# Kernel tuning notes

Hardware: AMD Instinct MI355X
Metric: run time of the kernel (lower is better)

The kernel has to match this reference:

```python
import jax, jax.numpy as jnp
import numpy as np

# Static per-expert capacities (tokens are laid out contiguously per expert)
CAPS = [1024, 512, 1024, 256, 1024, 512, 128, 1024, 512, 1024, 256, 512, 1024, 128, 64, 512]
TOTAL = sum(CAPS)  # 9536
E, H, I = 16, 1024, 4096
OFFSETS = np.concatenate([[0], np.cumsum(CAPS)])


def setup_inputs() -> dict:
    key = jax.random.key(0)
    ks = jax.random.split(key, 5)
    x = jax.random.normal(ks[0], (TOTAL, H), dtype=jnp.float32)
    W1 = jax.random.normal(ks[1], (E, I, H), dtype=jnp.float32) * 0.02
    b1 = jax.random.normal(ks[2], (E, I), dtype=jnp.float32) * 0.02
    W2 = jax.random.normal(ks[3], (E, H, I), dtype=jnp.float32) * 0.02
    b2 = jax.random.normal(ks[4], (E, H), dtype=jnp.float32) * 0.02
    return {"x": x, "W1": W1, "b1": b1, "W2": W2, "b2": b2}


def reference(x, W1, b1, W2, b2):
    # Grouped GEMM FFN: expert e processes rows [OFFSETS[e]:OFFSETS[e+1]]
    # out = gelu(x_e @ W1[e].T + b1[e]) @ W2[e].T + b2[e]
    outs = []
    for e in range(E):  # fixed, static loop over experts (capacities are static)
        xs = x[OFFSETS[e]:OFFSETS[e + 1]]                      # [cap_e, H]
        h = jax.nn.gelu(xs @ W1[e].T + b1[e], approximate=False)  # [cap_e, I]
        outs.append(h @ W2[e].T + b2[e])                       # [cap_e, H]
    return jnp.concatenate(outs, axis=0)                       # [TOTAL, H]
```

## Files before the change

kernel.cpp:

```cpp
#include <hip/hip_runtime.h>
#include <math.h>

typedef __attribute__((ext_vector_type(8))) short short8;
typedef __attribute__((ext_vector_type(4))) float f32x4;
typedef __attribute__((ext_vector_type(2))) unsigned int u32x2;

#define E_NUM 16
constexpr int CAPS[E_NUM] = {1024,512,1024,256,1024,512,128,1024,512,1024,256,512,1024,128,64,512};
constexpr int OFFS[E_NUM] = {0,1024,1536,2560,2816,3840,4352,4480,5504,6016,7040,7296,7808,8832,8960,9024};
constexpr int cdiv_(int a, int b){ return (a + b - 1) / b; }
constexpr int ilog2_(int v){ int l = 0; while ((1 << l) < v) ++l; return l; }

__device__ __forceinline__ unsigned int cvt_pk_bf16(float a, float b){
  unsigned int r;
  asm("v_cvt_pk_bf16_f32 %0, %1, %2" : "=v"(r) : "v"(a), "v"(b));
  return r;
}

typedef __attribute__((address_space(1))) const unsigned char gas_u8;
typedef __attribute__((address_space(3))) unsigned char las_u8;
__device__ __forceinline__ void gl_lds16(const void* g, void* l){
  __builtin_amdgcn_global_load_lds((gas_u8*)g, (las_u8*)l, 16, 0, 0);
}

__global__ __launch_bounds__(256) void cvt_bf16_kernel(const float* __restrict__ x,
                                                       unsigned short* __restrict__ xb, int n8)
{
  int i = blockIdx.x * blockDim.x + threadIdx.x;
  const int stride = gridDim.x * blockDim.x;
  for (; i < n8; i += stride) {
    f32x4 a = *reinterpret_cast<const f32x4*>(x + (size_t)i * 8);
    f32x4 b = *reinterpret_cast<const f32x4*>(x + (size_t)i * 8 + 4);
    u32x2 lo, hi;
    lo[0] = cvt_pk_bf16(a[0], a[1]); lo[1] = cvt_pk_bf16(a[2], a[3]);
    hi[0] = cvt_pk_bf16(b[0], b[1]); hi[1] = cvt_pk_bf16(b[2], b[3]);
    *reinterpret_cast<u32x2*>(xb + (size_t)i * 8)     = lo;
    *reinterpret_cast<u32x2*>(xb + (size_t)i * 8 + 4) = hi;
  }
}

template<bool A_GLDS, bool GELU_OUT, int TM, int NDIM, int KDIM, int LOG_GN, int NWG>
__global__ __launch_bounds__(256, 4)
void expert_gemm(const void* __restrict__ Av, const float* __restrict__ W,
                 const float* __restrict__ bias, void* __restrict__ Outv)
{
  constexpr int A_SZ = TM * 32;
  constexpr int B_SZ = 128 * 32;
  constexpr int GN   = 1 << LOG_GN;
  constexpr int MFR  = TM / 32;
  static_assert(NWG % 8 == 0, "grid must be divisible by 8 for XCD swizzle");
  static_assert(!GELU_OUT || 2 * (A_SZ + B_SZ) >= 128 * 128, "GELU transpose needs 32KB");

  __shared__ __align__(16) unsigned short smem[2 * A_SZ + 2 * B_SZ];

  const int tid  = threadIdx.x;
  const int braw = blockIdx.x;
  const int t = (braw & 7) * (NWG / 8) + (braw >> 3);

  int m0 = 0, n0 = 0, Me = 0, tok0 = 0;
  size_t wbase = 0, bbase = 0;
  {
    int acc0 = 0;
    #pragma unroll
    for (int i = 0; i < E_NUM; ++i) {
      const int mt  = cdiv_(CAPS[i], TM);
      const int lmt = ilog2_(mt);
      const int nb  = mt * (NDIM / 128);
      if (t >= acc0 && t < acc0 + nb) {
        const int loc = t - acc0;
        const int g   = loc >> (lmt + LOG_GN);
        const int rem = loc & ((mt << LOG_GN) - 1);
        m0   = (rem >> LOG_GN) * TM;
        n0   = ((g << LOG_GN) | (rem & (GN - 1))) * 128;
        Me   = CAPS[i];
        tok0 = OFFS[i];
        wbase = (size_t)i * NDIM * KDIM;
        bbase = (size_t)i * NDIM;
      }
      acc0 += nb;
    }
  }
  const float* Wb = W + wbase;

  const int lane = tid & 63;
  const int wv   = tid >> 6;
  const int sr   = tid >> 3;
  const int sc   = (tid & 7) * 8;
  const int spc  = sc ^ ((sr & 3) << 4);

  const unsigned short* Ah = (const unsigned short*)Av;
  const float*          Af = (const float*)Av;

  f32x4 ra[MFR]; f32x4 rb[4];

  auto loadB = [&](int kt) {
    const int k0 = kt * 32;
    #pragma unroll
    for (int i = 0; i < 4; ++i)
      rb[i] = *reinterpret_cast<const f32x4*>(Wb + (size_t)(n0 + sr + 32 * i) * KDIM + k0 + (sc >> 1));
  };
  auto writeB = [&](int buf) {
    char* bb = (char*)(smem + 2 * A_SZ + buf * B_SZ);
    #pragma unroll
    for (int i = 0; i < 4; ++i) {
      u32x2 p;
      p[0] = cvt_pk_bf16(rb[i][0], rb[i][1]);
      p[1] = cvt_pk_bf16(rb[i][2], rb[i][3]);
      *reinterpret_cast<u32x2*>(bb + (sr + 32 * i) * 64 + spc) = p;
    }
  };

  auto stageA_glds = [&](int buf, int kt) {
    constexpr int AI = TM / 64;
    const unsigned short* Ag = Ah + (size_t)(tok0 + m0) * KDIM + kt * 32;
    #pragma unroll
    for (int j = 0; j < AI; ++j) {
      const int rbase = wv * (AI * 16) + j * 16;
      const int r     = rbase + (lane >> 2);
      const int gblk  = (lane & 3) ^ (r & 3);
      gl_lds16((const void*)(Ag + (size_t)r * KDIM + gblk * 8),
               (void*)(smem + buf * A_SZ + rbase * 32));
    }
  };
  auto loadA_reg = [&](int kt) {
    const int k0 = kt * 32;
    #pragma unroll
    for (int i = 0; i < MFR; ++i)
      ra[i] = *reinterpret_cast<const f32x4*>(Af + (size_t)(tok0 + m0 + sr + 32 * i) * KDIM + k0 + (sc >> 1));
  };
  auto writeA_reg = [&](int buf) {
    char* ab = (char*)(smem + buf * A_SZ);
    #pragma unroll
    for (int i = 0; i < MFR; ++i) {
      u32x2 p;
      p[0] = cvt_pk_bf16(ra[i][0], ra[i][1]);
      p[1] = cvt_pk_bf16(ra[i][2], ra[i][3]);
      *reinterpret_cast<u32x2*>(ab + (sr + 32 * i) * 64 + spc) = p;
    }
  };

  const int wm   = (wv >> 1) * (TM / 2);
  const int wn   = (wv & 1) * 64;
  const int lrow = lane & 15;
  const int fcs  = ((lane >> 4) << 4) ^ ((lane & 3) << 4);

  f32x4 acc_[MFR][4];
  #pragma unroll
  for (int i = 0; i < MFR; ++i)
    #pragma unroll
    for (int j = 0; j < 4; ++j)
      acc_[i][j] = (f32x4){0.f, 0.f, 0.f, 0.f};

  loadB(0);
  if constexpr (A_GLDS) stageA_glds(0, 0); else { loadA_reg(0); writeA_reg(0); }
  writeB(0);
  __syncthreads();

  constexpr int NT = KDIM / 32;
  for (int kt = 0; kt < NT; ++kt) {
    const int cur = kt & 1;
    if (kt + 1 < NT) {
      loadB(kt + 1);
      if constexpr (A_GLDS) stageA_glds(cur ^ 1, kt + 1);
      else                  loadA_reg(kt + 1);
    }

    const char* ab = (const char*)(smem + cur * A_SZ);
    const char* bb = (const char*)(smem + 2 * A_SZ + cur * B_SZ);
    short8 afr[MFR], bfr[4];
    #pragma unroll
    for (int f = 0; f < MFR; ++f)
      afr[f] = *reinterpret_cast<const short8*>(ab + (wm + f * 16 + lrow) * 64 + fcs);
    #pragma unroll
    for (int f = 0; f < 4; ++f)
      bfr[f] = *reinterpret_cast<const short8*>(bb + (wn + f * 16 + lrow) * 64 + fcs);

    #pragma unroll
    for (int i = 0; i < MFR; ++i)
      #pragma unroll
      for (int j = 0; j < 4; ++j)
        acc_[i][j] = __builtin_amdgcn_mfma_f32_16x16x32_bf16(afr[i], bfr[j], acc_[i][j], 0, 0, 0);

    if (kt + 1 < NT) {
      writeB(cur ^ 1);
      if constexpr (!A_GLDS) writeA_reg(cur ^ 1);
    }
    __syncthreads();
  }

  float bv[4];
  #pragma unroll
  for (int f = 0; f < 4; ++f)
    bv[f] = bias[bbase + n0 + wn + f * 16 + lrow];

  if constexpr (GELU_OUT) {
    static_assert(TM == 128, "GELU path assumes 128-row tiles");
    unsigned short* hout = smem;
    #pragma unroll
    for (int i = 0; i < MFR; ++i) {
      const int rbase = wm + i * 16 + (lane >> 4) * 4;
      #pragma unroll
      for (int j = 0; j < 4; ++j) {
        #pragma unroll
        for (int jj = 0; jj < 4; ++jj) {
          float xv = acc_[i][j][jj] + bv[j];
          float g  = 0.5f * xv * (1.0f + erff(xv * 0.70710678118654752f));
          hout[(rbase + jj) * 128 + wn + j * 16 + lrow] = (unsigned short)(cvt_pk_bf16(g, g) & 0xFFFFu);
        }
      }
    }
    __syncthreads();
    unsigned short* Oh = (unsigned short*)Outv;
    #pragma unroll
    for (int it = 0; it < 8; ++it) {
      int row  = it * 16 + (tid >> 4);
      int c    = (tid & 15) * 8;
      int grow = m0 + row;
      if (grow < Me) {
        *reinterpret_cast<short8*>(Oh + (size_t)(tok0 + grow) * NDIM + n0 + c)
          = *reinterpret_cast<const short8*>(hout + row * 128 + c);
      }
    }
  } else {
    float* Of = (float*)Outv;
    #pragma unroll
    for (int i = 0; i < MFR; ++i) {
      const int rbase = wm + i * 16 + (lane >> 4) * 4;
      #pragma unroll
      for (int jj = 0; jj < 4; ++jj) {
        int grow = m0 + rbase + jj;
        if (grow < Me) {
          #pragma unroll
          for (int j = 0; j < 4; ++j) {
            Of[(size_t)(tok0 + grow) * NDIM + n0 + wn + j * 16 + lrow] = acc_[i][j][jj] + bv[j];
          }
        }
      }
    }
  }
}

extern "C" void kernel_launch(void* const* d_in, const int* in_sizes, int n_in,
                              void* d_out, int out_size, void* d_ws, size_t ws_size,
                              hipStream_t stream)
{
  const float* x  = (const float*)d_in[0];
  const float* W1 = (const float*)d_in[1];
  const float* b1 = (const float*)d_in[2];
  const float* W2 = (const float*)d_in[3];
  const float* b2 = (const float*)d_in[4];
  float* out = (float*)d_out;

  constexpr size_t H_BYTES  = (size_t)9536 * 4096 * 2;
  constexpr size_t XB_BYTES = (size_t)9536 * 1024 * 2;
  unsigned short* h  = (unsigned short*)d_ws;
  unsigned short* xb = (unsigned short*)((char*)d_ws + H_BYTES);

  const bool use_xb = ws_size >= H_BYTES + XB_BYTES;

  if (use_xb) {
    cvt_bf16_kernel<<<2048, 256, 0, stream>>>(x, xb, 9536 * 1024 / 8);
    expert_gemm<true, true, 128, 4096, 1024, 2, 75 * 32>
        <<<75 * 32, 256, 0, stream>>>((const void*)xb, W1, b1, (void*)h);
  } else {
    expert_gemm<false, true, 128, 4096, 1024, 2, 75 * 32>
        <<<75 * 32, 256, 0, stream>>>((const void*)x, W1, b1, (void*)h);
  }

  expert_gemm<true, false, 64, 1024, 4096, 0, 149 * 8>
      <<<149 * 8, 256, 0, stream>>>((const void*)h, W2, b2, (void*)out);
}
```

Measured before the change: 398.2 us.

## Split-K second expert GEMM with atomics and use cheaper sigmoid-form GELU

Splits the K dimension of the down-projection GEMM into two chunks processed by separate workgroups, accumulating into a zeroed output via atomic adds with the bias scaled per split. This raises the workgroup count to improve occupancy and load balance. It also replaces the erf-based GELU with a tanh-style approximation expressed as x*sigmoid, and raises the launch-bounds occupancy hint. The costs are an extra memset, atomic traffic, nondeterministic summation order, slightly approximate GELU, and possible register pressure.

Measured after the change: 403.5 us. No clear change (+1.3%).

```diff
diff --git a/kernel.cpp b/kernel.cpp
--- a/kernel.cpp
+++ b/kernel.cpp
@@ -39,8 +39,8 @@
   }
 }
 
-template<bool A_GLDS, bool GELU_OUT, int TM, int NDIM, int KDIM, int LOG_GN, int NWG>
-__global__ __launch_bounds__(256, 4)
+template<bool A_GLDS, bool GELU_OUT, int TM, int NDIM, int KDIM, int LOG_GN, int NWG, int KS>
+__global__ __launch_bounds__(256, 8)
 void expert_gemm(const void* __restrict__ Av, const float* __restrict__ W,
                  const float* __restrict__ bias, void* __restrict__ Outv)
 {
@@ -48,14 +48,21 @@
   constexpr int B_SZ = 128 * 32;
   constexpr int GN   = 1 << LOG_GN;
   constexpr int MFR  = TM / 32;
+  constexpr int NT   = KDIM / (KS * 32);
+  constexpr int NWG1 = NWG / KS;
   static_assert(NWG % 8 == 0, "grid must be divisible by 8 for XCD swizzle");
   static_assert(!GELU_OUT || 2 * (A_SZ + B_SZ) >= 128 * 128, "GELU transpose needs 32KB");
+  static_assert(!GELU_OUT || KS == 1, "GELU path is KS=1 only");
 
   __shared__ __align__(16) unsigned short smem[2 * A_SZ + 2 * B_SZ];
 
   const int tid  = threadIdx.x;
   const int braw = blockIdx.x;
   const int t = (braw & 7) * (NWG / 8) + (braw >> 3);
+
+  const int kc    = t / NWG1;
+  const int tt    = t % NWG1;
+  const int kbase = kc * (KDIM / KS);
 
   int m0 = 0, n0 = 0, Me = 0, tok0 = 0;
   size_t wbase = 0, bbase = 0;
@@ -66,8 +73,8 @@
       const int mt  = cdiv_(CAPS[i], TM);
       const int lmt = ilog2_(mt);
       const int nb  = mt * (NDIM / 128);
-      if (t >= acc0 && t < acc0 + nb) {
-        const int loc = t - acc0;
+      if (tt >= acc0 && tt < acc0 + nb) {
+        const int loc = tt - acc0;
         const int g   = loc >> (lmt + LOG_GN);
         const int rem = loc & ((mt << LOG_GN) - 1);
         m0   = (rem >> LOG_GN) * TM;
@@ -94,7 +101,7 @@
   f32x4 ra[MFR]; f32x4 rb[4];
 
   auto loadB = [&](int kt) {
-    const int k0 = kt * 32;
+    const int k0 = kbase + kt * 32;
     #pragma unroll
     for (int i = 0; i < 4; ++i)
       rb[i] = *reinterpret_cast<const f32x4*>(Wb + (size_t)(n0 + sr + 32 * i) * KDIM + k0 + (sc >> 1));
@@ -112,7 +119,7 @@
 
   auto stageA_glds = [&](int buf, int kt) {
     constexpr int AI = TM / 64;
-    const unsigned short* Ag = Ah + (size_t)(tok0 + m0) * KDIM + kt * 32;
+    const unsigned short* Ag = Ah + (size_t)(tok0 + m0) * KDIM + kbase + kt * 32;
     #pragma unroll
     for (int j = 0; j < AI; ++j) {
       const int rbase = wv * (AI * 16) + j * 16;
@@ -123,7 +130,7 @@
     }
   };
   auto loadA_reg = [&](int kt) {
-    const int k0 = kt * 32;
+    const int k0 = kbase + kt * 32;
     #pragma unroll
     for (int i = 0; i < MFR; ++i)
       ra[i] = *reinterpret_cast<const f32x4*>(Af + (size_t)(tok0 + m0 + sr + 32 * i) * KDIM + k0 + (sc >> 1));
@@ -151,12 +158,29 @@
     for (int j = 0; j < 4; ++j)
       acc_[i][j] = (f32x4){0.f, 0.f, 0.f, 0.f};
 
+  auto mfma_step = [&](int cur) {
+    const char* ab = (const char*)(smem + cur * A_SZ);
+    const char* bb = (const char*)(smem + 2 * A_SZ + cur * B_SZ);
+    short8 afr[MFR], bfr[4];
+    #pragma unroll
+    for (int f = 0; f < MFR; ++f)
+      afr[f] = *reinterpret_cast<const short8*>(ab + (wm + f * 16 + lrow) * 64 + fcs);
+    #pragma unroll
+    for (int f = 0; f < 4; ++f)
+      bfr[f] = *reinterpret_cast<const short8*>(bb + (wn + f * 16 + lrow) * 64 + fcs);
+    #pragma unroll
+    for (int i = 0; i < MFR; ++i)
+      #pragma unroll
+      for (int j = 0; j < 4; ++j)
+        acc_[i][j] = __builtin_amdgcn_mfma_f32_16x16x32_bf16(afr[i], bfr[j], acc_[i][j], 0, 0, 0);
+  };
+
   loadB(0);
-  if constexpr (A_GLDS) stageA_glds(0, 0); else { loadA_reg(0); writeA_reg(0); }
+  if constexpr (A_GLDS) stageA_glds(0, 0); else loadA_reg(0);
   writeB(0);
+  if constexpr (!A_GLDS) writeA_reg(0);
   __syncthreads();
 
-  constexpr int NT = KDIM / 32;
   for (int kt = 0; kt < NT; ++kt) {
     const int cur = kt & 1;
     if (kt + 1 < NT) {
@@ -164,23 +188,7 @@
       if constexpr (A_GLDS) stageA_glds(cur ^ 1, kt + 1);
       else                  loadA_reg(kt + 1);
     }
-
-    const char* ab = (const char*)(smem + cur * A_SZ);
-    const char* bb = (const char*)(smem + 2 * A_SZ + cur * B_SZ);
-    short8 afr[MFR], bfr[4];
-    #pragma unroll
-    for (int f = 0; f < MFR; ++f)
-      afr[f] = *reinterpret_cast<const short8*>(ab + (wm + f * 16 + lrow) * 64 + fcs);
-    #pragma unroll
-    for (int f = 0; f < 4; ++f)
-      bfr[f] = *reinterpret_cast<const short8*>(bb + (wn + f * 16 + lrow) * 64 + fcs);
-
-    #pragma unroll
-    for (int i = 0; i < MFR; ++i)
-      #pragma unroll
-      for (int j = 0; j < 4; ++j)
-        acc_[i][j] = __builtin_amdgcn_mfma_f32_16x16x32_bf16(afr[i], bfr[j], acc_[i][j], 0, 0, 0);
-
+    mfma_step(cur);
     if (kt + 1 < NT) {
       writeB(cur ^ 1);
       if constexpr (!A_GLDS) writeA_reg(cur ^ 1);
@@ -204,7 +212,8 @@
         #pragma unroll
         for (int jj = 0; jj < 4; ++jj) {
           float xv = acc_[i][j][jj] + bv[j];
-          float g  = 0.5f * xv * (1.0f + erff(xv * 0.70710678118654752f));
+          float y2 = xv * (1.5957691216057308f + 0.07135481627f * xv * xv);
+          float g  = xv * __builtin_amdgcn_rcpf(1.0f + __expf(-y2));
           hout[(rbase + jj) * 128 + wn + j * 16 + lrow] = (unsigned short)(cvt_pk_bf16(g, g) & 0xFFFFu);
         }
       }
@@ -223,6 +232,7 @@
     }
   } else {
     float* Of = (float*)Outv;
+    constexpr float BS = 1.0f / (float)KS;
     #pragma unroll
     for (int i = 0; i < MFR; ++i) {
       const int rbase = wm + i * 16 + (lane >> 4) * 4;
@@ -232,7 +242,10 @@
         if (grow < Me) {
           #pragma unroll
           for (int j = 0; j < 4; ++j) {
-            Of[(size_t)(tok0 + grow) * NDIM + n0 + wn + j * 16 + lrow] = acc_[i][j][jj] + bv[j];
+            float v = acc_[i][j][jj] + bv[j] * BS;
+            float* p = Of + (size_t)(tok0 + grow) * NDIM + n0 + wn + j * 16 + lrow;
+            if constexpr (KS > 1) unsafeAtomicAdd(p, v);
+            else                  *p = v;
           }
         }
       }
@@ -258,15 +271,17 @@
 
   const bool use_xb = ws_size >= H_BYTES + XB_BYTES;
 
+  hipMemsetAsync(d_out, 0, (size_t)out_size * sizeof(float), stream);
+
   if (use_xb) {
     cvt_bf16_kernel<<<2048, 256, 0, stream>>>(x, xb, 9536 * 1024 / 8);
-    expert_gemm<true, true, 128, 4096, 1024, 2, 75 * 32>
+    expert_gemm<true, true, 128, 4096, 1024, 2, 75 * 32, 1>
         <<<75 * 32, 256, 0, stream>>>((const void*)xb, W1, b1, (void*)h);
   } else {
-    expert_gemm<false, true, 128, 4096, 1024, 2, 75 * 32>
+    expert_gemm<false, true, 128, 4096, 1024, 2, 75 * 32, 1>
         <<<75 * 32, 256, 0, stream>>>((const void*)x, W1, b1, (void*)h);
   }
 
-  expert_gemm<true, false, 64, 1024, 4096, 0, 149 * 8>
-      <<<149 * 8, 256, 0, stream>>>((const void*)h, W2, b2, (void*)out);
-}
+  expert_gemm<true, false, 64, 1024, 4096, 0, 2 * 149 * 8, 2>
+      <<<2 * 149 * 8, 256, 0, stream>>>((const void*)h, W2, b2, (void*)out);
+}
```
